# Optimization experiments

Measured on AMD Instinct MI355X. Metric: run time of the kernel, lower is better.

The kernel has to match this reference:

```python
import jax, jax.numpy as jnp
import numpy as np

B, S = 4, 2048
N_EMBED = 1024
D_FF = 4 * N_EMBED
N_EXPERTS = 8
TOP_K = 2


def setup_inputs() -> dict:
    key = jax.random.key(0)
    ks = jax.random.split(key, 12)
    std = 0.02
    return {
        "x": jax.random.normal(ks[0], (B, S, N_EMBED), dtype=jnp.float32),
        "noise_u": jax.random.uniform(ks[1], (B, S, N_EXPERTS), dtype=jnp.float32),
        # router params
        "wg": jax.random.normal(ks[2], (N_EMBED, N_EXPERTS), dtype=jnp.float32) * std,
        "bg": jnp.zeros((N_EXPERTS,), dtype=jnp.float32),
        "wn": jax.random.normal(ks[3], (N_EMBED, N_EXPERTS), dtype=jnp.float32) * std,
        "bn": jnp.zeros((N_EXPERTS,), dtype=jnp.float32),
        # stacked expert params [E, ...]
        "w1": jax.random.normal(ks[4], (N_EXPERTS, N_EMBED, D_FF), dtype=jnp.float32) * std,
        "b1": jnp.zeros((N_EXPERTS, D_FF), dtype=jnp.float32),
        "w2": jax.random.normal(ks[5], (N_EXPERTS, D_FF, N_EMBED), dtype=jnp.float32) * std,
        "b2": jnp.zeros((N_EXPERTS, N_EMBED), dtype=jnp.float32),
    }


def reference(x, noise_u, wg, bg, wn, bn, w1, b1, w2, b2):
    # ---- NoisyTopKRouter ----
    logits = x @ wg + bg                              # [B,S,E]
    noise_logits = x @ wn + bn                        # [B,S,E]
    noisy = logits + noise_u * jax.nn.softplus(noise_logits)
    top_vals, top_idx = jax.lax.top_k(noisy, TOP_K)   # [B,S,K]
    # selected-expert mask; scatter of top-k logits == where(selected, noisy, -inf)
    sel = jax.nn.one_hot(top_idx, N_EXPERTS).sum(axis=-2) > 0   # [B,S,E] bool
    sparse_logits = jnp.where(sel, noisy, -jnp.inf)
    gates = jax.nn.softmax(sparse_logits, axis=-1)    # zero for unselected experts
    # ---- per-expert MLP, combined with gate weights (zero gate => no contribution) ----
    out = jnp.zeros_like(x)
    for e in range(N_EXPERTS):
        h = jax.nn.relu(x @ w1[e] + b1[e])            # [B,S,4d]
        y = h @ w2[e] + b2[e]                         # [B,S,d]
        out = out + gates[..., e:e + 1] * y
    return out
```

## Files before the change

kernel.cpp:

```cpp
#include <hip/hip_runtime.h>
#include <hip/hip_bf16.h>


#define T_TOK 8192
#define D_EMB 1024
#define DFF   4096
#define N_EXP 8
#define BM 128
#define BN 128
#define BK 64

typedef __attribute__((ext_vector_type(8))) short bf16x8;
typedef __attribute__((ext_vector_type(4))) float floatx4;
typedef unsigned short bf16_t;

__device__ __forceinline__ bf16_t f2bf(float f) {
  union { float f; unsigned u; } a; a.f = f;
  unsigned u = a.u;
  return (bf16_t)((u + 0x7fffu + ((u >> 16) & 1u)) >> 16);
}

__global__ __launch_bounds__(256) void cvt_x_k(const float* __restrict__ x,
                                               bf16_t* __restrict__ xb) {
  int i = (blockIdx.x * 256 + threadIdx.x) * 4;
  float4 v = *(const float4*)(x + i);
  ushort4 o;
  o.x = f2bf(v.x); o.y = f2bf(v.y); o.z = f2bf(v.z); o.w = f2bf(v.w);
  *(ushort4*)(xb + i) = o;
}

__global__ __launch_bounds__(256) void tcvt_k(const float* __restrict__ in,
                                              bf16_t* __restrict__ outp,
                                              int K, int N) {
  __shared__ float tile[32][33];
  int e  = blockIdx.z;
  int n0 = blockIdx.x * 32;
  int k0 = blockIdx.y * 32;
  int tx = threadIdx.x;
  int ty = threadIdx.y;
  const float* src = in + (size_t)e * K * N;
#pragma unroll
  for (int l = 0; l < 32; l += 8)
    tile[ty + l][tx] = src[(size_t)(k0 + ty + l) * N + (n0 + tx)];
  __syncthreads();
  bf16_t* dst = outp + (size_t)e * K * N;
#pragma unroll
  for (int l = 0; l < 32; l += 8)
    dst[(size_t)(n0 + ty + l) * K + (k0 + tx)] = f2bf(tile[tx][ty + l]);
}

__global__ __launch_bounds__(256) void router_k(
    const float* __restrict__ x, const float* __restrict__ nu,
    const float* __restrict__ wg, const float* __restrict__ bgp,
    const float* __restrict__ wn, const float* __restrict__ bnp,
    int* __restrict__ cnt, int* __restrict__ tok, float* __restrict__ gate) {
  int t = blockIdx.x;
  int tid = threadIdx.x;
  float gl[8] = {0,0,0,0,0,0,0,0};
  float nl[8] = {0,0,0,0,0,0,0,0};
  const float* xr = x + (size_t)t * D_EMB;
  for (int i = tid; i < D_EMB; i += 256) {
    float xv = xr[i];
    float4 a0 = *(const float4*)(wg + i * 8);
    float4 a1 = *(const float4*)(wg + i * 8 + 4);
    float4 c0 = *(const float4*)(wn + i * 8);
    float4 c1 = *(const float4*)(wn + i * 8 + 4);
    gl[0] += xv * a0.x; gl[1] += xv * a0.y; gl[2] += xv * a0.z; gl[3] += xv * a0.w;
    gl[4] += xv * a1.x; gl[5] += xv * a1.y; gl[6] += xv * a1.z; gl[7] += xv * a1.w;
    nl[0] += xv * c0.x; nl[1] += xv * c0.y; nl[2] += xv * c0.z; nl[3] += xv * c0.w;
    nl[4] += xv * c1.x; nl[5] += xv * c1.y; nl[6] += xv * c1.z; nl[7] += xv * c1.w;
  }
  __shared__ float red[4][16];
  int lane = tid & 63;
  int wv = tid >> 6;
#pragma unroll
  for (int o = 0; o < 16; ++o) {
    float v = (o < 8) ? gl[o] : nl[o - 8];
#pragma unroll
    for (int s = 32; s > 0; s >>= 1) v += __shfl_down(v, s, 64);
    if (lane == 0) red[wv][o] = v;
  }
  __syncthreads();
  if (tid == 0) {
    float noisy[8];
#pragma unroll
    for (int e = 0; e < 8; ++e) {
      float lg = red[0][e] + red[1][e] + red[2][e] + red[3][e] + bgp[e];
      float nz = red[0][8 + e] + red[1][8 + e] + red[2][8 + e] + red[3][8 + e] + bnp[e];
      float sp = fmaxf(nz, 0.f) + log1pf(expf(-fabsf(nz)));
      noisy[e] = lg + nu[(size_t)t * 8 + e] * sp;
    }
    int e1 = 0;
#pragma unroll
    for (int e = 1; e < 8; ++e) if (noisy[e] > noisy[e1]) e1 = e;
    int e2 = -1;
#pragma unroll
    for (int e = 0; e < 8; ++e) {
      if (e == e1) continue;
      if (e2 < 0 || noisy[e] > noisy[e2]) e2 = e;
    }
    float d = expf(noisy[e2] - noisy[e1]);
    float g1 = 1.f / (1.f + d);
    float g2 = d / (1.f + d);
    int p1 = atomicAdd(&cnt[e1], 1);
    tok[e1 * T_TOK + p1] = t; gate[e1 * T_TOK + p1] = g1;
    int p2 = atomicAdd(&cnt[e2], 1);
    tok[e2 * T_TOK + p2] = t; gate[e2 * T_TOK + p2] = g2;
  }
}

__global__ void scan_k(const int* __restrict__ cnt, int* __restrict__ offs) {
  if (threadIdx.x == 0 && blockIdx.x == 0) {
    int a = 0;
    for (int e = 0; e < N_EXP; ++e) { offs[e] = a; a += cnt[e]; }
    offs[N_EXP] = a;
  }
}

__global__ __launch_bounds__(256) void gemm1_k(
    const bf16_t* __restrict__ xb, const bf16_t* __restrict__ w1T,
    const float* __restrict__ b1p, const int* __restrict__ cnt,
    const int* __restrict__ offs, const int* __restrict__ tok,
    bf16_t* __restrict__ h) {
  const int NT = DFF / BN;
  const int MT = T_TOK / BM;
  int bid = blockIdx.x;
  int e = bid / (MT * NT);
  int rem = bid % (MT * NT);
  int mt = rem / NT;
  int nt = rem % NT;
  int cnte = cnt[e];
  if (mt * BM >= cnte) return;
  int rows = min(BM, cnte - mt * BM);

  __shared__ bf16_t As[BM][BK + 8];
  __shared__ bf16_t Bs[BN][BK + 8];
  __shared__ int stok[BM];

  int tid = threadIdx.x;
  if (tid < BM) {
    int r = mt * BM + ((tid < rows) ? tid : 0);
    stok[tid] = tok[e * T_TOK + r];
  }
  __syncthreads();

  int lane = tid & 63;
  int wv = tid >> 6;
  int m0 = (wv & 1) * 64;
  int n0 = (wv >> 1) * 64;
  int lm = lane & 15;
  int lq = lane >> 4;

  floatx4 acc[4][4];
#pragma unroll
  for (int i = 0; i < 4; ++i)
#pragma unroll
    for (int j = 0; j < 4; ++j)
#pragma unroll
      for (int r = 0; r < 4; ++r) acc[i][j][r] = 0.f;

  int srow = tid >> 1;
  int soff = (tid & 1) * 32;
  size_t arow = (size_t)stok[srow] * D_EMB + soff;
  const bf16_t* wbase = w1T + ((size_t)e * DFF + nt * BN + srow) * D_EMB + soff;

  for (int kk = 0; kk < D_EMB; kk += BK) {
    const uint4* ga = (const uint4*)(xb + arow + kk);
    const uint4* gb = (const uint4*)(wbase + kk);
    uint4 a0 = ga[0], a1 = ga[1], a2 = ga[2], a3 = ga[3];
    uint4 b0 = gb[0], b1v = gb[1], b2v = gb[2], b3v = gb[3];
    uint4* la = (uint4*)&As[srow][soff];
    uint4* lb = (uint4*)&Bs[srow][soff];
    la[0] = a0; la[1] = a1; la[2] = a2; la[3] = a3;
    lb[0] = b0; lb[1] = b1v; lb[2] = b2v; lb[3] = b3v;
    __syncthreads();
#pragma unroll
    for (int ks = 0; ks < BK; ks += 32) {
      bf16x8 af[4], bfr[4];
#pragma unroll
      for (int i = 0; i < 4; ++i)
        af[i] = *(const bf16x8*)&As[m0 + i * 16 + lm][ks + lq * 8];
#pragma unroll
      for (int j = 0; j < 4; ++j)
        bfr[j] = *(const bf16x8*)&Bs[n0 + j * 16 + lm][ks + lq * 8];
#pragma unroll
      for (int i = 0; i < 4; ++i)
#pragma unroll
        for (int j = 0; j < 4; ++j)
          acc[i][j] = __builtin_amdgcn_mfma_f32_16x16x32_bf16(af[i], bfr[j], acc[i][j], 0, 0, 0);
    }
    __syncthreads();
  }

  int hbase = offs[e] + mt * BM;
#pragma unroll
  for (int i = 0; i < 4; ++i) {
    int lr0 = m0 + i * 16 + lq * 4;
#pragma unroll
    for (int r = 0; r < 4; ++r) {
      if (lr0 + r < rows) {
        size_t hrow = (size_t)(hbase + lr0 + r) * DFF;
#pragma unroll
        for (int j = 0; j < 4; ++j) {
          int col = nt * BN + n0 + j * 16 + lm;
          float v = acc[i][j][r] + b1p[e * DFF + col];
          h[hrow + col] = f2bf(fmaxf(v, 0.f));
        }
      }
    }
  }
}

__global__ __launch_bounds__(256) void gemm2_k(
    const bf16_t* __restrict__ h, const bf16_t* __restrict__ w2T,
    const float* __restrict__ b2p, const int* __restrict__ cnt,
    const int* __restrict__ offs, const int* __restrict__ tok,
    const float* __restrict__ gate, float* __restrict__ out) {
  const int NT = D_EMB / BN;
  const int MT = T_TOK / BM;
  int bid = blockIdx.x;
  int e = bid / (MT * NT);
  int rem = bid % (MT * NT);
  int mt = rem / NT;
  int nt = rem % NT;
  int cnte = cnt[e];
  if (mt * BM >= cnte) return;
  int rows = min(BM, cnte - mt * BM);

  __shared__ bf16_t As[BM][BK + 8];
  __shared__ bf16_t Bs[BN][BK + 8];
  __shared__ int stok[BM];
  __shared__ float sgate[BM];

  int tid = threadIdx.x;
  if (tid < BM) {
    int idx = e * T_TOK + mt * BM + ((tid < rows) ? tid : 0);
    stok[tid] = tok[idx];
    sgate[tid] = gate[idx];
  }
  __syncthreads();

  int lane = tid & 63;
  int wv = tid >> 6;
  int m0 = (wv & 1) * 64;
  int n0 = (wv >> 1) * 64;
  int lm = lane & 15;
  int lq = lane >> 4;

  floatx4 acc[4][4];
#pragma unroll
  for (int i = 0; i < 4; ++i)
#pragma unroll
    for (int j = 0; j < 4; ++j)
#pragma unroll
      for (int r = 0; r < 4; ++r) acc[i][j][r] = 0.f;

  int srow = tid >> 1;
  int soff = (tid & 1) * 32;
  int srow_c = (srow < rows) ? srow : 0;
  const bf16_t* abase = h + ((size_t)(offs[e] + mt * BM + srow_c)) * DFF + soff;
  const bf16_t* wbase = w2T + ((size_t)e * D_EMB + nt * BN + srow) * DFF + soff;

  for (int kk = 0; kk < DFF; kk += BK) {
    const uint4* ga = (const uint4*)(abase + kk);
    const uint4* gb = (const uint4*)(wbase + kk);
    uint4 a0 = ga[0], a1 = ga[1], a2 = ga[2], a3 = ga[3];
    uint4 b0 = gb[0], b1v = gb[1], b2v = gb[2], b3v = gb[3];
    uint4* la = (uint4*)&As[srow][soff];
    uint4* lb = (uint4*)&Bs[srow][soff];
    la[0] = a0; la[1] = a1; la[2] = a2; la[3] = a3;
    lb[0] = b0; lb[1] = b1v; lb[2] = b2v; lb[3] = b3v;
    __syncthreads();
#pragma unroll
    for (int ks = 0; ks < BK; ks += 32) {
      bf16x8 af[4], bfr[4];
#pragma unroll
      for (int i = 0; i < 4; ++i)
        af[i] = *(const bf16x8*)&As[m0 + i * 16 + lm][ks + lq * 8];
#pragma unroll
      for (int j = 0; j < 4; ++j)
        bfr[j] = *(const bf16x8*)&Bs[n0 + j * 16 + lm][ks + lq * 8];
#pragma unroll
      for (int i = 0; i < 4; ++i)
#pragma unroll
        for (int j = 0; j < 4; ++j)
          acc[i][j] = __builtin_amdgcn_mfma_f32_16x16x32_bf16(af[i], bfr[j], acc[i][j], 0, 0, 0);
    }
    __syncthreads();
  }

#pragma unroll
  for (int i = 0; i < 4; ++i) {
    int lr0 = m0 + i * 16 + lq * 4;
#pragma unroll
    for (int r = 0; r < 4; ++r) {
      int lr = lr0 + r;
      if (lr < rows) {
        int t = stok[lr];
        float g = sgate[lr];
#pragma unroll
        for (int j = 0; j < 4; ++j) {
          int col = nt * BN + n0 + j * 16 + lm;
          float v = g * (acc[i][j][r] + b2p[e * D_EMB + col]);
          unsafeAtomicAdd(&out[(size_t)t * D_EMB + col], v);
        }
      }
    }
  }
}

extern "C" void kernel_launch(void* const* d_in, const int* in_sizes, int n_in,
                              void* d_out, int out_size, void* d_ws, size_t ws_size,
                              hipStream_t stream) {
  const float* x  = (const float*)d_in[0];
  const float* nu = (const float*)d_in[1];
  const float* wg = (const float*)d_in[2];
  const float* bg = (const float*)d_in[3];
  const float* wn = (const float*)d_in[4];
  const float* bn = (const float*)d_in[5];
  const float* w1 = (const float*)d_in[6];
  const float* b1 = (const float*)d_in[7];
  const float* w2 = (const float*)d_in[8];
  const float* b2 = (const float*)d_in[9];
  float* out = (float*)d_out;

  char* ws = (char*)d_ws;
  size_t o = 0;
  int* cnt  = (int*)(ws + o);
  int* offs = cnt + 8;
  o += 256;
  int*   tok  = (int*)(ws + o);   o += (size_t)N_EXP * T_TOK * 4;
  float* gate = (float*)(ws + o); o += (size_t)N_EXP * T_TOK * 4;
  bf16_t* xb  = (bf16_t*)(ws + o); o += (size_t)T_TOK * D_EMB * 2;
  bf16_t* w1T = (bf16_t*)(ws + o); o += (size_t)N_EXP * D_EMB * DFF * 2;
  bf16_t* w2T = (bf16_t*)(ws + o); o += (size_t)N_EXP * D_EMB * DFF * 2;
  bf16_t* h   = (bf16_t*)(ws + o); o += (size_t)2 * T_TOK * DFF * 2;
  (void)o; (void)ws_size; (void)in_sizes; (void)n_in;

  hipMemsetAsync(cnt, 0, 256, stream);
  hipMemsetAsync(out, 0, (size_t)out_size * sizeof(float), stream);

  cvt_x_k<<<(T_TOK * D_EMB) / 1024, 256, 0, stream>>>(x, xb);
  tcvt_k<<<dim3(DFF / 32, D_EMB / 32, N_EXP), dim3(32, 8), 0, stream>>>(w1, w1T, D_EMB, DFF);
  tcvt_k<<<dim3(D_EMB / 32, DFF / 32, N_EXP), dim3(32, 8), 0, stream>>>(w2, w2T, DFF, D_EMB);
  router_k<<<T_TOK, 256, 0, stream>>>(x, nu, wg, bg, wn, bn, cnt, tok, gate);
  scan_k<<<1, 64, 0, stream>>>(cnt, offs);
  gemm1_k<<<N_EXP * (T_TOK / BM) * (DFF / BN), 256, 0, stream>>>(xb, w1T, b1, cnt, offs, tok, h);
  gemm2_k<<<N_EXP * (T_TOK / BM) * (D_EMB / BN), 256, 0, stream>>>(h, w2T, b2, cnt, offs, tok, gate, out);
}
```

Measured before the change: 1.064 ms.

## Use direct global-to-LDS loads in expert GEMMs, fuse x conversion into router

The expert GEMM tile loads now go straight from global memory into LDS with global_load_lds, bypassing registers. The LDS padding is removed so the 16-byte-per-lane row layout matches what the direct-load path expects. The bf16 conversion of x is folded into the router kernel, which removes a separate pass over x. The weight transpose-convert kernel is widened to 64x64 tiles with float4 reads and 16-byte writes. Dropping the LDS padding can bring back bank conflicts on the MFMA fragment reads. One sync in gemm2 was removed, so the first reads of stok/sgate may now rely on the loop barrier.

```diff
diff --git a/kernel.cpp b/kernel.cpp
--- a/kernel.cpp
+++ b/kernel.cpp
@@ -20,47 +20,56 @@
   return (bf16_t)((u + 0x7fffu + ((u >> 16) & 1u)) >> 16);
 }
 
-__global__ __launch_bounds__(256) void cvt_x_k(const float* __restrict__ x,
-                                               bf16_t* __restrict__ xb) {
-  int i = (blockIdx.x * 256 + threadIdx.x) * 4;
-  float4 v = *(const float4*)(x + i);
-  ushort4 o;
-  o.x = f2bf(v.x); o.y = f2bf(v.y); o.z = f2bf(v.z); o.w = f2bf(v.w);
-  *(ushort4*)(xb + i) = o;
+__device__ __forceinline__ void ld_lds16(const bf16_t* g, bf16_t* l) {
+  __builtin_amdgcn_global_load_lds(
+      (const __attribute__((address_space(1))) void*)g,
+      (__attribute__((address_space(3))) void*)l, 16, 0, 0);
 }
 
 __global__ __launch_bounds__(256) void tcvt_k(const float* __restrict__ in,
                                               bf16_t* __restrict__ outp,
                                               int K, int N) {
-  __shared__ float tile[32][33];
-  int e  = blockIdx.z;
-  int n0 = blockIdx.x * 32;
-  int k0 = blockIdx.y * 32;
-  int tx = threadIdx.x;
-  int ty = threadIdx.y;
+  __shared__ bf16_t t[64][72];
+  int e = blockIdx.z, n0 = blockIdx.x * 64, k0 = blockIdx.y * 64;
+  int tid = threadIdx.x;
   const float* src = in + (size_t)e * K * N;
-#pragma unroll
-  for (int l = 0; l < 32; l += 8)
-    tile[ty + l][tx] = src[(size_t)(k0 + ty + l) * N + (n0 + tx)];
+  int kr = tid >> 4;
+  int nc = (tid & 15) * 4;
+#pragma unroll
+  for (int p = 0; p < 4; ++p) {
+    int k = p * 16 + kr;
+    float4 v = *(const float4*)(src + (size_t)(k0 + k) * N + n0 + nc);
+    t[nc + 0][k] = f2bf(v.x);
+    t[nc + 1][k] = f2bf(v.y);
+    t[nc + 2][k] = f2bf(v.z);
+    t[nc + 3][k] = f2bf(v.w);
+  }
   __syncthreads();
   bf16_t* dst = outp + (size_t)e * K * N;
-#pragma unroll
-  for (int l = 0; l < 32; l += 8)
-    dst[(size_t)(n0 + ty + l) * K + (k0 + tx)] = f2bf(tile[tx][ty + l]);
+  int nr = tid >> 3;
+  int kc = (tid & 7) * 8;
+#pragma unroll
+  for (int p = 0; p < 2; ++p) {
+    int n = p * 32 + nr;
+    *(uint4*)(dst + (size_t)(n0 + n) * K + k0 + kc) = *(const uint4*)&t[n][kc];
+  }
 }
 
 __global__ __launch_bounds__(256) void router_k(
     const float* __restrict__ x, const float* __restrict__ nu,
     const float* __restrict__ wg, const float* __restrict__ bgp,
     const float* __restrict__ wn, const float* __restrict__ bnp,
-    int* __restrict__ cnt, int* __restrict__ tok, float* __restrict__ gate) {
+    int* __restrict__ cnt, int* __restrict__ tok, float* __restrict__ gate,
+    bf16_t* __restrict__ xb) {
   int t = blockIdx.x;
   int tid = threadIdx.x;
   float gl[8] = {0,0,0,0,0,0,0,0};
   float nl[8] = {0,0,0,0,0,0,0,0};
   const float* xr = x + (size_t)t * D_EMB;
+  bf16_t* xbr = xb + (size_t)t * D_EMB;
   for (int i = tid; i < D_EMB; i += 256) {
     float xv = xr[i];
+    xbr[i] = f2bf(xv);
     float4 a0 = *(const float4*)(wg + i * 8);
     float4 a1 = *(const float4*)(wg + i * 8 + 4);
     float4 c0 = *(const float4*)(wn + i * 8);
@@ -133,19 +142,30 @@
   if (mt * BM >= cnte) return;
   int rows = min(BM, cnte - mt * BM);
 
-  __shared__ bf16_t As[BM][BK + 8];
-  __shared__ bf16_t Bs[BN][BK + 8];
+  __shared__ bf16_t As[BM][BK];
+  __shared__ bf16_t Bs[BN][BK];
   __shared__ int stok[BM];
 
   int tid = threadIdx.x;
   if (tid < BM) {
-    int r = mt * BM + ((tid < rows) ? tid : 0);
+    int r = mt * BM + ((tid < rows) ? tid : rows - 1);
     stok[tid] = tok[e * T_TOK + r];
   }
   __syncthreads();
 
   int lane = tid & 63;
   int wv = tid >> 6;
+  int srow8 = lane >> 3;
+  int schunk = (lane & 7) * 8;
+  const bf16_t* aptr[4];
+  const bf16_t* bptr[4];
+#pragma unroll
+  for (int it = 0; it < 4; ++it) {
+    int r = wv * 32 + it * 8 + srow8;
+    aptr[it] = xb + (size_t)stok[r] * D_EMB + schunk;
+    bptr[it] = w1T + ((size_t)e * DFF + nt * BN + r) * D_EMB + schunk;
+  }
+
   int m0 = (wv & 1) * 64;
   int n0 = (wv >> 1) * 64;
   int lm = lane & 15;
@@ -159,20 +179,12 @@
 #pragma unroll
       for (int r = 0; r < 4; ++r) acc[i][j][r] = 0.f;
 
-  int srow = tid >> 1;
-  int soff = (tid & 1) * 32;
-  size_t arow = (size_t)stok[srow] * D_EMB + soff;
-  const bf16_t* wbase = w1T + ((size_t)e * DFF + nt * BN + srow) * D_EMB + soff;
-
   for (int kk = 0; kk < D_EMB; kk += BK) {
-    const uint4* ga = (const uint4*)(xb + arow + kk);
-    const uint4* gb = (const uint4*)(wbase + kk);
-    uint4 a0 = ga[0], a1 = ga[1], a2 = ga[2], a3 = ga[3];
-    uint4 b0 = gb[0], b1v = gb[1], b2v = gb[2], b3v = gb[3];
-    uint4* la = (uint4*)&As[srow][soff];
-    uint4* lb = (uint4*)&Bs[srow][soff];
-    la[0] = a0; la[1] = a1; la[2] = a2; la[3] = a3;
-    lb[0] = b0; lb[1] = b1v; lb[2] = b2v; lb[3] = b3v;
+#pragma unroll
+    for (int it = 0; it < 4; ++it) {
+      ld_lds16(aptr[it] + kk, &As[wv * 32 + it * 8][0]);
+      ld_lds16(bptr[it] + kk, &Bs[wv * 32 + it * 8][0]);
+    }
     __syncthreads();
 #pragma unroll
     for (int ks = 0; ks < BK; ks += 32) {
@@ -227,8 +239,8 @@
   if (mt * BM >= cnte) return;
   int rows = min(BM, cnte - mt * BM);
 
-  __shared__ bf16_t As[BM][BK + 8];
-  __shared__ bf16_t Bs[BN][BK + 8];
+  __shared__ bf16_t As[BM][BK];
+  __shared__ bf16_t Bs[BN][BK];
   __shared__ int stok[BM];
   __shared__ float sgate[BM];
 
@@ -238,10 +250,22 @@
     stok[tid] = tok[idx];
     sgate[tid] = gate[idx];
   }
-  __syncthreads();
 
   int lane = tid & 63;
   int wv = tid >> 6;
+  int srow8 = lane >> 3;
+  int schunk = (lane & 7) * 8;
+  int hbase0 = offs[e] + mt * BM;
+  const bf16_t* aptr[4];
+  const bf16_t* bptr[4];
+#pragma unroll
+  for (int it = 0; it < 4; ++it) {
+    int r = wv * 32 + it * 8 + srow8;
+    int rc = (r < rows) ? r : 0;
+    aptr[it] = h + (size_t)(hbase0 + rc) * DFF + schunk;
+    bptr[it] = w2T + ((size_t)e * D_EMB + nt * BN + r) * DFF + schunk;
+  }
+
   int m0 = (wv & 1) * 64;
   int n0 = (wv >> 1) * 64;
   int lm = lane & 15;
@@ -255,21 +279,12 @@
 #pragma unroll
       for (int r = 0; r < 4; ++r) acc[i][j][r] = 0.f;
 
-  int srow = tid >> 1;
-  int soff = (tid & 1) * 32;
-  int srow_c = (srow < rows) ? srow : 0;
-  const bf16_t* abase = h + ((size_t)(offs[e] + mt * BM + srow_c)) * DFF + soff;
-  const bf16_t* wbase = w2T + ((size_t)e * D_EMB + nt * BN + srow) * DFF + soff;
-
   for (int kk = 0; kk < DFF; kk += BK) {
-    const uint4* ga = (const uint4*)(abase + kk);
-    const uint4* gb = (const uint4*)(wbase + kk);
-    uint4 a0 = ga[0], a1 = ga[1], a2 = ga[2], a3 = ga[3];
-    uint4 b0 = gb[0], b1v = gb[1], b2v = gb[2], b3v = gb[3];
-    uint4* la = (uint4*)&As[srow][soff];
-    uint4* lb = (uint4*)&Bs[srow][soff];
-    la[0] = a0; la[1] = a1; la[2] = a2; la[3] = a3;
-    lb[0] = b0; lb[1] = b1v; lb[2] = b2v; lb[3] = b3v;
+#pragma unroll
+    for (int it = 0; it < 4; ++it) {
+      ld_lds16(aptr[it] + kk, &As[wv * 32 + it * 8][0]);
+      ld_lds16(bptr[it] + kk, &Bs[wv * 32 + it * 8][0]);
+    }
     __syncthreads();
 #pragma unroll
     for (int ks = 0; ks < BK; ks += 32) {
@@ -340,10 +355,9 @@
   hipMemsetAsync(cnt, 0, 256, stream);
   hipMemsetAsync(out, 0, (size_t)out_size * sizeof(float), stream);
 
-  cvt_x_k<<<(T_TOK * D_EMB) / 1024, 256, 0, stream>>>(x, xb);
-  tcvt_k<<<dim3(DFF / 32, D_EMB / 32, N_EXP), dim3(32, 8), 0, stream>>>(w1, w1T, D_EMB, DFF);
-  tcvt_k<<<dim3(D_EMB / 32, DFF / 32, N_EXP), dim3(32, 8), 0, stream>>>(w2, w2T, DFF, D_EMB);
-  router_k<<<T_TOK, 256, 0, stream>>>(x, nu, wg, bg, wn, bn, cnt, tok, gate);
+  tcvt_k<<<dim3(DFF / 64, D_EMB / 64, N_EXP), 256, 0, stream>>>(w1, w1T, D_EMB, DFF);
+  tcvt_k<<<dim3(D_EMB / 64, DFF / 64, N_EXP), 256, 0, stream>>>(w2, w2T, DFF, D_EMB);
+  router_k<<<T_TOK, 256, 0, stream>>>(x, nu, wg, bg, wn, bn, cnt, tok, gate, xb);
   scan_k<<<1, 64, 0, stream>>>(cnt, offs);
   gemm1_k<<<N_EXP * (T_TOK / BM) * (DFF / BN), 256, 0, stream>>>(xb, w1T, b1, cnt, offs, tok, h);
   gemm2_k<<<N_EXP * (T_TOK / BM) * (D_EMB / BN), 256, 0, stream>>>(h, w2T, b2, cnt, offs, tok, gate, out);
```

Measured after the change: 1.185 ms. 11.4% more time.
